# Performance work log

Measured on AMD Instinct MI355X. Metric: run time of the kernel, lower is better.

The kernel has to match this reference:

```python
import jax, jax.numpy as jnp
import numpy as np

OUT_H, OUT_W = 7, 7
SPATIAL_SCALE = 1.0  # aligned=True (align_corners=True interpolate), per init_kwargs


def setup_inputs() -> dict:
    key = jax.random.key(0)
    kf, kb, kx, ky, kw, kh = jax.random.split(key, 6)
    B, C, H, W = 4, 256, 200, 200
    N = 512
    features = jax.random.normal(kf, (B, C, H, W), dtype=jnp.float32)
    batch_idx = jax.random.randint(kb, (N,), 0, B, dtype=jnp.int32)
    # integer boxes with x2>x1, y2>y1, strictly inside the map
    x1 = jax.random.randint(kx, (N,), 0, W - 64, dtype=jnp.int32)
    y1 = jax.random.randint(ky, (N,), 0, H - 64, dtype=jnp.int32)
    bw = jax.random.randint(kw, (N,), 8, 64, dtype=jnp.int32)
    bh = jax.random.randint(kh, (N,), 8, 64, dtype=jnp.int32)
    x2 = jnp.minimum(x1 + bw, W - 1)
    y2 = jnp.minimum(y1 + bh, H - 1)
    rois = jnp.stack([batch_idx, x1, y1, x2, y2], axis=1)  # [N, 5] int32
    return {"features": features, "rois": rois}


def reference(features, rois):
    # features: [B, C, H, W]; rois: [N, 5] int32 (batch, x1, y1, x2, y2)
    # Faithful to: crop features[b, :, y1:y2+1, x1:x2+1] then
    # F.interpolate(size=(7,7), mode='bilinear', align_corners=True).
    N = rois.shape[0]
    H, W = features.shape[2], features.shape[3]
    b = rois[:, 0]
    coords = rois[:, 1:5].astype(jnp.float32) * SPATIAL_SCALE
    x1, y1, x2, y2 = coords[:, 0], coords[:, 1], coords[:, 2], coords[:, 3]

    # align_corners=True source coords inside the crop, offset into the full map
    jy = jnp.arange(OUT_H, dtype=jnp.float32)
    jx = jnp.arange(OUT_W, dtype=jnp.float32)
    sy = y1[:, None] + jy[None, :] * (y2 - y1)[:, None] / (OUT_H - 1)  # [N, OH]
    sx = x1[:, None] + jx[None, :] * (x2 - x1)[:, None] / (OUT_W - 1)  # [N, OW]

    y0f = jnp.floor(sy); x0f = jnp.floor(sx)
    wy = sy - y0f                                  # [N, OH]
    wx = sx - x0f                                  # [N, OW]
    y0 = jnp.clip(y0f.astype(jnp.int32), 0, H - 1)
    y1i = jnp.clip(y0 + 1, 0, H - 1)
    x0 = jnp.clip(x0f.astype(jnp.int32), 0, W - 1)
    x1i = jnp.clip(x0 + 1, 0, W - 1)

    bb = b[:, None, None]                          # [N,1,1]

    def gather(yi, xi):
        # advanced indexing -> [N, OH, OW, C]
        return features[bb, :, yi[:, :, None], xi[:, None, :]]

    v00 = gather(y0, x0)
    v01 = gather(y0, x1i)
    v10 = gather(y1i, x0)
    v11 = gather(y1i, x1i)

    wyb = wy[:, :, None, None]                     # [N, OH, 1, 1]
    wxb = wx[:, None, :, None]                     # [N, 1, OW, 1]
    out = (v00 * (1 - wyb) * (1 - wxb) + v01 * (1 - wyb) * wxb
           + v10 * wyb * (1 - wxb) + v11 * wyb * wxb)  # [N, OH, OW, C]
    return jnp.transpose(out, (0, 3, 1, 2))        # [N, C, OH, OW]
```

## Files before the change

kernel.cpp:

```cpp
#include <hip/hip_runtime.h>

#define OUT_H 7
#define OUT_W 7

#define FEAT_H 200
#define FEAT_W 200

__global__ __launch_bounds__(256) void roialign_kernel(
    const float* __restrict__ feat,
    const int*   __restrict__ rois,
    float*       __restrict__ out,
    int N, int C, int total)
{
    int idx = blockIdx.x * blockDim.x + threadIdx.x;
    if (idx >= total) return;

    const int H = FEAT_H, W = FEAT_W;

    int jx = idx % OUT_W;
    int t  = idx / OUT_W;
    int jy = t % OUT_H;
    t /= OUT_H;
    int c = t % C;
    int n = t / C;

    const int* r = rois + n * 5;
    int b = r[0];
    float x1 = (float)r[1];
    float y1 = (float)r[2];
    float x2 = (float)r[3];
    float y2 = (float)r[4];

    float sy = y1 + ((float)jy * (y2 - y1)) / (float)(OUT_H - 1);
    float sx = x1 + ((float)jx * (x2 - x1)) / (float)(OUT_W - 1);

    float y0f = floorf(sy);
    float x0f = floorf(sx);
    float wy = sy - y0f;
    float wx = sx - x0f;

    int y0  = min(max((int)y0f, 0), H - 1);
    int y1i = min(y0 + 1, H - 1);
    int x0  = min(max((int)x0f, 0), W - 1);
    int x1i = min(x0 + 1, W - 1);

    const float* fp = feat + ((size_t)b * C + c) * (size_t)(H * W);
    float v00 = fp[y0  * W + x0 ];
    float v01 = fp[y0  * W + x1i];
    float v10 = fp[y1i * W + x0 ];
    float v11 = fp[y1i * W + x1i];

    float omwy = 1.0f - wy;
    float omwx = 1.0f - wx;
    out[idx] = v00 * omwy * omwx + v01 * omwy * wx
             + v10 * wy   * omwx + v11 * wy   * wx;
}

extern "C" void kernel_launch(void* const* d_in, const int* in_sizes, int n_in,
                              void* d_out, int out_size, void* d_ws, size_t ws_size,
                              hipStream_t stream)
{
    const float* feat = (const float*)d_in[0];
    const int*   rois = (const int*)d_in[1];
    float*       out  = (float*)d_out;

    int N = in_sizes[1] / 5;
    int C = out_size / (N * OUT_H * OUT_W);
    int total = out_size;

    int threads = 256;
    int blocks = (total + threads - 1) / threads;
    roialign_kernel<<<blocks, threads, 0, stream>>>(feat, rois, out, N, C, total);
}
```

Measured before the change: 261.2 us.

## Transpose features to NHWC in workspace, then gather channels coalesced per ROI

A tiled transpose kernel first converts the NCHW feature map to NHWC in the workspace buffer. A second kernel then runs one block per ROI, with threads mapped to channels, so each bilinear sample reads contiguous channel vectors. Results are staged in shared memory and written out coalesced in NCHW order. This trades a full read and write of the feature map for removing the scattered, poorly coalesced gathers of the original per-output kernel. It falls back to the direct kernel when the workspace is too small or C is not 256.

```diff
diff --git a/kernel.cpp b/kernel.cpp
--- a/kernel.cpp
+++ b/kernel.cpp
@@ -2,56 +2,128 @@
 
 #define OUT_H 7
 #define OUT_W 7
-
 #define FEAT_H 200
 #define FEAT_W 200
+#define TILE 32
 
-__global__ __launch_bounds__(256) void roialign_kernel(
-    const float* __restrict__ feat,
+__global__ __launch_bounds__(256) void nchw_to_nhwc(
+    const float* __restrict__ in,
+    float* __restrict__ out,
+    int C, int HW)
+{
+    __shared__ float tile[TILE][TILE + 1];
+    int hw0 = blockIdx.x * TILE;
+    int c0  = blockIdx.y * TILE;
+    int b   = blockIdx.z;
+    const float* inb = in + (size_t)b * C * HW;
+    float* outb      = out + (size_t)b * HW * C;
+    int tx = threadIdx.x, ty = threadIdx.y;
+
+#pragma unroll
+    for (int i = 0; i < 4; ++i) {
+        int c  = c0 + ty + i * 8;
+        int hw = hw0 + tx;
+        if (c < C && hw < HW)
+            tile[ty + i * 8][tx] = inb[(size_t)c * HW + hw];
+    }
+    __syncthreads();
+#pragma unroll
+    for (int i = 0; i < 4; ++i) {
+        int hw = hw0 + ty + i * 8;
+        int c  = c0 + tx;
+        if (c < C && hw < HW)
+            outb[(size_t)hw * C + c] = tile[tx][ty + i * 8];
+    }
+}
+
+__global__ __launch_bounds__(256) void roialign_nhwc(
+    const float* __restrict__ featT,
     const int*   __restrict__ rois,
     float*       __restrict__ out,
-    int N, int C, int total)
+    int C)
+{
+    __shared__ float acc[256 * OUT_H * OUT_W];
+    const int H = FEAT_H, W = FEAT_W;
+    int n = blockIdx.x;
+    int c = threadIdx.x;
+
+    const int* r = rois + n * 5;
+    int   b   = r[0];
+    float x1f = (float)r[1];
+    float y1f = (float)r[2];
+    float dx  = (float)r[3] - x1f;
+    float dy  = (float)r[4] - y1f;
+
+    const float* fb = featT + (size_t)b * (H * W) * C + c;
+
+    for (int jy = 0; jy < OUT_H; ++jy) {
+        float sy   = y1f + ((float)jy * dy) / (float)(OUT_H - 1);
+        float y0fl = floorf(sy);
+        float wy   = sy - y0fl;
+        int y0  = min(max((int)y0fl, 0), H - 1);
+        int y1i = min(y0 + 1, H - 1);
+        float omwy = 1.0f - wy;
+        const float* row0 = fb + (size_t)(y0  * W) * C;
+        const float* row1 = fb + (size_t)(y1i * W) * C;
+
+#pragma unroll
+        for (int jx = 0; jx < OUT_W; ++jx) {
+            float sx   = x1f + ((float)jx * dx) / (float)(OUT_W - 1);
+            float x0fl = floorf(sx);
+            float wx   = sx - x0fl;
+            int x0  = min(max((int)x0fl, 0), W - 1);
+            int x1i = min(x0 + 1, W - 1);
+            float omwx = 1.0f - wx;
+
+            float v00 = row0[(size_t)x0  * C];
+            float v01 = row0[(size_t)x1i * C];
+            float v10 = row1[(size_t)x0  * C];
+            float v11 = row1[(size_t)x1i * C];
+
+            acc[c * (OUT_H * OUT_W) + jy * OUT_W + jx] =
+                v00 * omwy * omwx + v01 * omwy * wx +
+                v10 * wy   * omwx + v11 * wy   * wx;
+        }
+    }
+    __syncthreads();
+
+    float* ob = out + (size_t)n * C * (OUT_H * OUT_W);
+    int total = C * OUT_H * OUT_W;
+    for (int k = c; k < total; k += blockDim.x)
+        ob[k] = acc[k];
+}
+
+__global__ __launch_bounds__(256) void roialign_direct(
+    const float* __restrict__ feat, const int* __restrict__ rois,
+    float* __restrict__ out, int C, int total)
 {
     int idx = blockIdx.x * blockDim.x + threadIdx.x;
     if (idx >= total) return;
-
     const int H = FEAT_H, W = FEAT_W;
-
     int jx = idx % OUT_W;
     int t  = idx / OUT_W;
     int jy = t % OUT_H;
     t /= OUT_H;
     int c = t % C;
     int n = t / C;
-
     const int* r = rois + n * 5;
     int b = r[0];
-    float x1 = (float)r[1];
-    float y1 = (float)r[2];
-    float x2 = (float)r[3];
-    float y2 = (float)r[4];
-
+    float x1 = (float)r[1], y1 = (float)r[2];
+    float x2 = (float)r[3], y2 = (float)r[4];
     float sy = y1 + ((float)jy * (y2 - y1)) / (float)(OUT_H - 1);
     float sx = x1 + ((float)jx * (x2 - x1)) / (float)(OUT_W - 1);
-
-    float y0f = floorf(sy);
-    float x0f = floorf(sx);
-    float wy = sy - y0f;
-    float wx = sx - x0f;
-
+    float y0f = floorf(sy), x0f = floorf(sx);
+    float wy = sy - y0f, wx = sx - x0f;
     int y0  = min(max((int)y0f, 0), H - 1);
     int y1i = min(y0 + 1, H - 1);
     int x0  = min(max((int)x0f, 0), W - 1);
     int x1i = min(x0 + 1, W - 1);
-
     const float* fp = feat + ((size_t)b * C + c) * (size_t)(H * W);
     float v00 = fp[y0  * W + x0 ];
     float v01 = fp[y0  * W + x1i];
     float v10 = fp[y1i * W + x0 ];
     float v11 = fp[y1i * W + x1i];
-
-    float omwy = 1.0f - wy;
-    float omwx = 1.0f - wx;
+    float omwy = 1.0f - wy, omwx = 1.0f - wx;
     out[idx] = v00 * omwy * omwx + v01 * omwy * wx
              + v10 * wy   * omwx + v11 * wy   * wx;
 }
@@ -64,11 +136,20 @@
     const int*   rois = (const int*)d_in[1];
     float*       out  = (float*)d_out;
 
-    int N = in_sizes[1] / 5;
-    int C = out_size / (N * OUT_H * OUT_W);
-    int total = out_size;
+    int N  = in_sizes[1] / 5;
+    int C  = out_size / (N * OUT_H * OUT_W);
+    int HW = FEAT_H * FEAT_W;
+    int B  = in_sizes[0] / (C * HW);
 
-    int threads = 256;
-    int blocks = (total + threads - 1) / threads;
-    roialign_kernel<<<blocks, threads, 0, stream>>>(feat, rois, out, N, C, total);
+    size_t need = (size_t)B * HW * C * sizeof(float);
+    if (ws_size >= need && C == 256) {
+        float* featT = (float*)d_ws;
+        dim3 tgrid((HW + TILE - 1) / TILE, (C + TILE - 1) / TILE, B);
+        dim3 tblk(32, 8, 1);
+        nchw_to_nhwc<<<tgrid, tblk, 0, stream>>>(feat, featT, C, HW);
+        roialign_nhwc<<<N, 256, 0, stream>>>(featT, rois, out, C);
+    } else {
+        int total = out_size;
+        roialign_direct<<<(total + 255) / 256, 256, 0, stream>>>(feat, rois, out, C, total);
+    }
 }
```

Measured after the change: 290.1 us. 11.1% more time.

## Stage ROI row spans in LDS per output row and interpolate from shared memory

Applied to the files above, without the earlier changes.

Replaces the one-thread-per-output gather kernel with a block per (ROI, output row). Each block cooperatively loads the two needed feature rows across the ROI's x-span for 64 channels at a time into LDS, then computes the 7 horizontal samples from shared memory. The goal is contiguous row loads instead of scattered 4-point gathers, at the cost of loading the whole x-span, extra barriers, and only 3584 blocks. Output writes become strided per channel rather than fully coalesced, and a fallback direct kernel handles non-default shapes.

```diff
diff --git a/kernel.cpp b/kernel.cpp
--- a/kernel.cpp
+++ b/kernel.cpp
@@ -2,56 +2,125 @@
 
 #define OUT_H 7
 #define OUT_W 7
-
 #define FEAT_H 200
 #define FEAT_W 200
+#define HW_ALL (FEAT_H * FEAT_W)
+#define CH 64
+#define LS 67
 
-__global__ __launch_bounds__(256) void roialign_kernel(
+__global__ __launch_bounds__(256) void roialign_fused(
     const float* __restrict__ feat,
     const int*   __restrict__ rois,
     float*       __restrict__ out,
-    int N, int C, int total)
+    int N)
+{
+    __shared__ float lds[2 * CH * LS];
+
+    int n  = blockIdx.x / OUT_H;
+    int jy = blockIdx.x % OUT_H;
+
+    const int* r = rois + n * 5;
+    int   b   = r[0];
+    float x1f = (float)r[1];
+    float y1f = (float)r[2];
+    float dx  = (float)r[3] - x1f;
+    float dy  = (float)r[4] - y1f;
+
+    float sy   = y1f + ((float)jy * dy) / 6.0f;
+    float y0fl = floorf(sy);
+    float wy   = sy - y0fl;
+    int y0  = min(max((int)y0fl, 0), FEAT_H - 1);
+    int y1i = min(y0 + 1, FEAT_H - 1);
+    float omwy = 1.0f - wy;
+
+    int xs = min(max((int)floorf(x1f), 0), FEAT_W - 1);
+    int xe = min((int)floorf(x1f + dx) + 1, FEAT_W - 1);
+    int wspan = xe - xs + 1;
+
+    int t    = threadIdx.x;
+    int wave = t >> 6;
+    int lane = t & 63;
+    int c    = t & 63;
+    int slot = t >> 6;
+
+    int yrow[2];
+    yrow[0] = y0;
+    yrow[1] = y1i;
+
+    size_t cbase = (size_t)b * 256 * HW_ALL;
+
+    for (int cg = 0; cg < 4; ++cg) {
+        __syncthreads();
+        for (int rr = wave; rr < 2 * CH; rr += 4) {
+            int yy = rr >> 6;
+            int cc = rr & 63;
+            const float* src = feat + cbase
+                             + (size_t)(cg * CH + cc) * HW_ALL
+                             + yrow[yy] * FEAT_W + xs;
+            float* dst = &lds[rr * LS];
+            if (lane < wspan) dst[lane] = src[lane];
+            int xt = 64 + lane;
+            if (xt < wspan) dst[xt] = src[xt];
+        }
+        __syncthreads();
+
+        const float* l0 = &lds[c * LS];
+        const float* l1 = &lds[(CH + c) * LS];
+        float* ob = out + (((size_t)n * 256 + cg * CH + c) * OUT_H + jy) * OUT_W;
+
+#pragma unroll
+        for (int j = 0; j < 2; ++j) {
+            int jx = slot + (j << 2);
+            if (jx < OUT_W) {
+                float sx   = x1f + ((float)jx * dx) / 6.0f;
+                float x0fl = floorf(sx);
+                float wx   = sx - x0fl;
+                int x0  = min(max((int)x0fl, 0), FEAT_W - 1);
+                int x1i = min(x0 + 1, FEAT_W - 1);
+                float omwx = 1.0f - wx;
+                int xi0 = x0  - xs;
+                int xi1 = x1i - xs;
+
+                float v00 = l0[xi0], v01 = l0[xi1];
+                float v10 = l1[xi0], v11 = l1[xi1];
+
+                ob[jx] = v00 * (omwy * omwx) + v01 * (omwy * wx)
+                       + v10 * (wy   * omwx) + v11 * (wy   * wx);
+            }
+        }
+    }
+}
+
+__global__ __launch_bounds__(256) void roialign_direct(
+    const float* __restrict__ feat, const int* __restrict__ rois,
+    float* __restrict__ out, int C, int H, int W, int total)
 {
     int idx = blockIdx.x * blockDim.x + threadIdx.x;
     if (idx >= total) return;
-
-    const int H = FEAT_H, W = FEAT_W;
-
     int jx = idx % OUT_W;
     int t  = idx / OUT_W;
     int jy = t % OUT_H;
     t /= OUT_H;
     int c = t % C;
     int n = t / C;
-
     const int* r = rois + n * 5;
     int b = r[0];
-    float x1 = (float)r[1];
-    float y1 = (float)r[2];
-    float x2 = (float)r[3];
-    float y2 = (float)r[4];
-
+    float x1 = (float)r[1], y1 = (float)r[2];
+    float x2 = (float)r[3], y2 = (float)r[4];
     float sy = y1 + ((float)jy * (y2 - y1)) / (float)(OUT_H - 1);
     float sx = x1 + ((float)jx * (x2 - x1)) / (float)(OUT_W - 1);
-
-    float y0f = floorf(sy);
-    float x0f = floorf(sx);
-    float wy = sy - y0f;
-    float wx = sx - x0f;
-
+    float y0f = floorf(sy), x0f = floorf(sx);
+    float wy = sy - y0f, wx = sx - x0f;
     int y0  = min(max((int)y0f, 0), H - 1);
     int y1i = min(y0 + 1, H - 1);
     int x0  = min(max((int)x0f, 0), W - 1);
     int x1i = min(x0 + 1, W - 1);
-
     const float* fp = feat + ((size_t)b * C + c) * (size_t)(H * W);
     float v00 = fp[y0  * W + x0 ];
     float v01 = fp[y0  * W + x1i];
     float v10 = fp[y1i * W + x0 ];
     float v11 = fp[y1i * W + x1i];
-
-    float omwy = 1.0f - wy;
-    float omwx = 1.0f - wx;
+    float omwy = 1.0f - wy, omwx = 1.0f - wx;
     out[idx] = v00 * omwy * omwx + v01 * omwy * wx
              + v10 * wy   * omwx + v11 * wy   * wx;
 }
@@ -64,11 +133,15 @@
     const int*   rois = (const int*)d_in[1];
     float*       out  = (float*)d_out;
 
-    int N = in_sizes[1] / 5;
-    int C = out_size / (N * OUT_H * OUT_W);
-    int total = out_size;
+    int N  = in_sizes[1] / 5;
+    int C  = out_size / (N * OUT_H * OUT_W);
+    int B  = in_sizes[0] / (C * HW_ALL);
 
-    int threads = 256;
-    int blocks = (total + threads - 1) / threads;
-    roialign_kernel<<<blocks, threads, 0, stream>>>(feat, rois, out, N, C, total);
+    if (C == 256 && in_sizes[0] == B * 256 * HW_ALL && B >= 1) {
+        roialign_fused<<<N * OUT_H, 256, 0, stream>>>(feat, rois, out, N);
+    } else {
+        int H = FEAT_H, W = FEAT_W;
+        int total = out_size;
+        roialign_direct<<<(total + 255) / 256, 256, 0, stream>>>(feat, rois, out, C, H, W, total);
+    }
 }
```

New measurement: 477.3 us. 82.8% more time.
